# Kernel optimization log

Measured on AMD Instinct MI355X. Metric: run time of the kernel, lower is better.

Reference implementation:

```python
import jax, jax.numpy as jnp
import numpy as np

HEADS = 4
DIM_HEAD = 128


def setup_inputs() -> dict:
    key = jax.random.key(0)
    k1, k2, k3, k4 = jax.random.split(key, 4)
    b, dim, H, W = 4, 256, 128, 128
    hidden = HEADS * DIM_HEAD  # 512
    x = jax.random.normal(k1, (b, dim, H, W), dtype=jnp.float32)
    # 1x1 convs are pointwise matmuls over channels
    w_qkv = jax.random.normal(k2, (hidden * 3, dim), dtype=jnp.float32) * 0.02
    w_out = jax.random.normal(k3, (dim, hidden), dtype=jnp.float32) * 0.02
    b_out = jax.random.normal(k4, (dim,), dtype=jnp.float32) * 0.02
    return {"x": x, "w_qkv": w_qkv, "w_out": w_out, "b_out": b_out}


def reference(x, w_qkv, w_out, b_out):
    b, c, h, w = x.shape
    n = h * w
    # to_qkv: 1x1 conv (no bias) == channel matmul -> [b, 3*heads*dh, h, w]
    qkv = jnp.einsum('bchw,oc->bohw', x, w_qkv)
    # 'b (qkv heads d) h w -> qkv b heads d (h w)'
    qkv = qkv.reshape(b, 3, HEADS, DIM_HEAD, n)
    q, k, v = qkv[:, 0], qkv[:, 1], qkv[:, 2]  # each [b, heads, d, n]
    k = jax.nn.softmax(k, axis=-1)  # softmax over spatial positions
    context = jnp.einsum('bhdn,bhen->bhde', k, v)   # [b, heads, d, d]
    out = jnp.einsum('bhde,bhdn->bhen', context, q)  # [b, heads, d, n]
    out = out.reshape(b, HEADS * DIM_HEAD, h, w)
    # to_out: 1x1 conv with bias
    return jnp.einsum('bchw,oc->bohw', out, w_out) + b_out[None, :, None, None]
```

## Files before the change

### kernel.cpp

```cpp
#include <hip/hip_runtime.h>
#include <hip/hip_bf16.h>

#define HEADS 4
#define DH    128
#define CIN   256
#define NPIX  16384
#define NB    4
#define HID   512

typedef __attribute__((ext_vector_type(8))) short bf16x8;
typedef __attribute__((ext_vector_type(4))) float f32x4;

__device__ __forceinline__ unsigned short f2bfu(float f) {
    union { __hip_bfloat16 h; unsigned short u; } cv;
    cv.h = __float2bfloat16(f);
    return cv.u;
}

typedef const __attribute__((address_space(1))) unsigned char* gas_t;
typedef __attribute__((address_space(3))) unsigned char* las_t;
__device__ __forceinline__ void glds16(const void* g, void* s) {
    __builtin_amdgcn_global_load_lds((gas_t)g, (las_t)s, 16, 0, 0);
}


__global__ __launch_bounds__(256) void xt_convert2(const float* __restrict__ x,
                                                   unsigned short* __restrict__ xt2,
                                                   unsigned short* __restrict__ xbf2)
{
    __shared__ float tile[64][66];
    const int b = blockIdx.z, c0 = blockIdx.y * 64, n0 = blockIdx.x * 64;
    const int t = threadIdx.x, lane = t & 63, wid = t >> 6;
    const float* xb = x + ((size_t)b * CIN + c0) * NPIX + n0;
#pragma unroll
    for (int p = 0; p < 4; ++p) {
        const int c = p * 16 + (t >> 4);
        const int n = (t & 15) * 4;
        float4 v = *reinterpret_cast<const float4*>(xb + (size_t)c * NPIX + n);
        tile[c][n + 0] = v.x; tile[c][n + 1] = v.y;
        tile[c][n + 2] = v.z; tile[c][n + 3] = v.w;
    }
    __syncthreads();
#pragma unroll
    for (int rr = 0; rr < 2; ++rr) {
        const int tid  = wid * 2 + rr;
        const int n16l = tid >> 1, c32l = tid & 1;
        const int nl   = n16l * 16 + (lane & 15);
        const int cb   = c32l * 32 + (lane >> 4) * 8;
        unsigned short u8[8];
#pragma unroll
        for (int j = 0; j < 8; ++j) u8[j] = f2bfu(tile[cb + j][nl]);
        *reinterpret_cast<uint4*>(
            xt2 + (((size_t)b * 1024 + (n0 >> 4) + n16l) * 8 + (c0 >> 5) + c32l) * 512 + lane * 8)
            = *reinterpret_cast<const uint4*>(u8);
    }
#pragma unroll
    for (int rr = 0; rr < 2; ++rr) {
        const int tid  = wid * 2 + rr;
        const int c16l = tid >> 1, n32l = tid & 1;
        const int cr   = c16l * 16 + (lane & 15);
        const int nb   = n32l * 32 + (lane >> 4) * 8;
        unsigned short u8[8];
#pragma unroll
        for (int j = 0; j < 8; ++j) u8[j] = f2bfu(tile[cr][nb + j]);
        *reinterpret_cast<uint4*>(
            xbf2 + (((size_t)b * 16 + (c0 >> 4) + c16l) * 512 + (n0 >> 5) + n32l) * 512 + lane * 8)
            = *reinterpret_cast<const uint4*>(u8);
    }
}

__global__ __launch_bounds__(256) void wconv3(const float* __restrict__ w_qkv,
                                              const float* __restrict__ w_out,
                                              unsigned short* __restrict__ WkF,
                                              unsigned short* __restrict__ WvF,
                                              unsigned short* __restrict__ WqTF,
                                              unsigned short* __restrict__ WoF)
{
    const int t = threadIdx.x, lane = t & 63, wid = t >> 6;
    const int tile = blockIdx.x * 4 + wid;
    unsigned short u8[8];
    unsigned short* dst;
    if (tile < 256) {
        const int h = tile >> 6, d16 = (tile >> 3) & 7, c32 = tile & 7;
        const float* src = w_qkv + (size_t)(512 + h * 128 + d16 * 16 + (lane & 15)) * CIN
                         + c32 * 32 + (lane >> 4) * 8;
#pragma unroll
        for (int j = 0; j < 8; ++j) u8[j] = f2bfu(src[j]);
        dst = WkF + (size_t)tile * 512 + lane * 8;
    } else if (tile < 512) {
        const int t2 = tile - 256;
        const int h = t2 >> 6, e16 = (t2 >> 3) & 7, c32 = t2 & 7;
        const float* src = w_qkv + (size_t)(1024 + h * 128 + e16 * 16 + (lane & 15)) * CIN
                         + c32 * 32 + (lane >> 4) * 8;
#pragma unroll
        for (int j = 0; j < 8; ++j) u8[j] = f2bfu(src[j]);
        dst = WvF + (size_t)t2 * 512 + lane * 8;
    } else if (tile < 768) {
        const int t2 = tile - 512;
        const int h = t2 >> 6, c16 = (t2 >> 2) & 15, d32 = t2 & 3;
#pragma unroll
        for (int j = 0; j < 8; ++j)
            u8[j] = f2bfu(w_qkv[(size_t)(h * 128 + d32 * 32 + (lane >> 4) * 8 + j) * CIN
                                + c16 * 16 + (lane & 15)]);
        dst = WqTF + (size_t)t2 * 512 + lane * 8;
    } else {
        const int t2 = tile - 768;
        const int o16 = t2 >> 4, m32 = t2 & 15;
        const float* src = w_out + (size_t)(o16 * 16 + (lane & 15)) * HID
                         + m32 * 32 + (lane >> 4) * 8;
#pragma unroll
        for (int j = 0; j < 8; ++j) u8[j] = f2bfu(src[j]);
        dst = WoF + (size_t)t2 * 512 + lane * 8;
    }
    *reinterpret_cast<uint4*>(dst) = *reinterpret_cast<const uint4*>(u8);
}

__global__ __launch_bounds__(512, 4) void kg_fused4(const unsigned short* __restrict__ xt2,
                                                    const unsigned short* __restrict__ xbf2,
                                                    const unsigned short* __restrict__ WkF,
                                                    float* __restrict__ G,
                                                    float* __restrict__ S)
{
    __shared__ unsigned short sXT[2][16 * 512];
    __shared__ unsigned short sXB[2][16 * 512];
    __shared__ unsigned short sP[4 * 512];

    const int t = threadIdx.x, lane = t & 63, wid = t >> 6;
    const int ns = blockIdx.x, hd = blockIdx.y, b = blockIdx.z;
    const int h = hd >> 1, dh = hd & 1;
    const int bh = b * 4 + h;
    const int wm = wid >> 1, wn = wid & 1;
    const int wd = wid >> 2, wcq = wid & 3;
    const int cl = lane & 15, r0q = (lane >> 4) * 4;

    bf16x8 aW[8];
#pragma unroll
    for (int ks = 0; ks < 8; ++ks)
        aW[ks] = *reinterpret_cast<const bf16x8*>(
            WkF + ((size_t)((h * 8 + dh * 4 + wm) * 8 + ks)) * 512 + lane * 8);

    f32x4 accG[2][4] = {};
    float Sacc[4] = {};

#define STAGE(nt_, buf_)                                                          \
    {                                                                             \
        _Pragma("unroll")                                                         \
        for (int q = 0; q < 2; ++q) {                                             \
            const int tl = wid * 2 + q;                                           \
            glds16(xt2 + (((size_t)(b * 1024 + ns * 64 + (nt_) * 2 + (tl >> 3))) * 8 \
                          + (tl & 7)) * 512 + lane * 8,                           \
                   sXT[buf_] + (size_t)tl * 512);                                 \
        }                                                                         \
        _Pragma("unroll")                                                         \
        for (int q = 0; q < 2; ++q) {                                             \
            const int tl = wid * 2 + q;                                           \
            glds16(xbf2 + (((size_t)(b * 16 + tl)) * 512 + ns * 32 + (nt_)) * 512 \
                          + lane * 8,                                             \
                   sXB[buf_] + (size_t)tl * 512);                                 \
        }                                                                         \
    }

    STAGE(0, 0);
    __syncthreads();

    int cur = 0;
    for (int nt = 0; nt < 32; ++nt) {
        if (nt < 31) STAGE(nt + 1, cur ^ 1);

        f32x4 acc1 = {};
#pragma unroll
        for (int ks = 0; ks < 8; ++ks) {
            bf16x8 bb = *reinterpret_cast<const bf16x8*>(
                &sXT[cur][(wn * 8 + ks) * 512 + lane * 8]);
            acc1 = __builtin_amdgcn_mfma_f32_16x16x32_bf16(aW[ks], bb, acc1, 0, 0, 0);
        }

#pragma unroll
        for (int r = 0; r < 4; ++r) {
            const float v = __expf(acc1[r]);
            Sacc[r] += v;
            const int us = ((r0q + r) + 16 * (wn * 2 + (cl >> 3))) * 8 + (cl & 7);
            sP[wm * 512 + us] = f2bfu(v);
        }
        __syncthreads();

        {
            const bf16x8 pa0 = *reinterpret_cast<const bf16x8*>(&sP[(wd * 2 + 0) * 512 + lane * 8]);
            const bf16x8 pa1 = *reinterpret_cast<const bf16x8*>(&sP[(wd * 2 + 1) * 512 + lane * 8]);
#pragma unroll
            for (int fj = 0; fj < 4; ++fj) {
                const bf16x8 bb = *reinterpret_cast<const bf16x8*>(
                    &sXB[cur][(wcq * 4 + fj) * 512 + lane * 8]);
                accG[0][fj] = __builtin_amdgcn_mfma_f32_16x16x32_bf16(pa0, bb, accG[0][fj], 0, 0, 0);
                accG[1][fj] = __builtin_amdgcn_mfma_f32_16x16x32_bf16(pa1, bb, accG[1][fj], 0, 0, 0);
            }
        }
        __syncthreads();
        cur ^= 1;
    }
#undef STAGE

#pragma unroll
    for (int r = 0; r < 4; ++r) {
        float v = Sacc[r];
        v += __shfl_xor(v, 1); v += __shfl_xor(v, 2);
        v += __shfl_xor(v, 4); v += __shfl_xor(v, 8);
        if (cl == 0)
            atomicAdd(&S[bh * 128 + dh * 64 + wm * 16 + r0q + r], v);
    }

#pragma unroll
    for (int fi = 0; fi < 2; ++fi)
#pragma unroll
        for (int fj = 0; fj < 4; ++fj)
#pragma unroll
            for (int r = 0; r < 4; ++r) {
                const int d = dh * 64 + wd * 32 + fi * 16 + r0q + r;
                const int c = wcq * 64 + fj * 16 + cl;
                atomicAdd(&G[(size_t)bh * 32768 + d * 256 + c], accG[fi][fj][r]);
            }
}

__global__ __launch_bounds__(256) void c1_kernel(const float* __restrict__ G,
                                                 const float* __restrict__ S,
                                                 const unsigned short* __restrict__ WvF,
                                                 const unsigned short* __restrict__ WqTF,
                                                 unsigned short* __restrict__ AbarF)
{
    __shared__ unsigned short sCtx[32 * 512];
    const int t = threadIdx.x, lane = t & 63, wid = t >> 6;
    const int bh = blockIdx.x, b = bh >> 2, h = bh & 3;
    const int cl = lane & 15, r0q = (lane >> 4) * 4;
    const int wr = wid >> 1, wc = wid & 1;
    const float* Gb = G + (size_t)bh * 32768;

    float invs[4];
#pragma unroll
    for (int fi = 0; fi < 4; ++fi)
        invs[fi] = 1.0f / S[bh * 128 + wr * 64 + fi * 16 + cl];

    f32x4 acc[4][4] = {};
#pragma unroll
    for (int ks = 0; ks < 8; ++ks) {
        bf16x8 a[4], bb[4];
#pragma unroll
        for (int fi = 0; fi < 4; ++fi) {
            const float* gp = Gb + (size_t)(wr * 64 + fi * 16 + cl) * 256
                            + ks * 32 + (lane >> 4) * 8;
            const float4 v0 = *reinterpret_cast<const float4*>(gp);
            const float4 v1 = *reinterpret_cast<const float4*>(gp + 4);
            unsigned short u8[8] = {
                f2bfu(v0.x * invs[fi]), f2bfu(v0.y * invs[fi]),
                f2bfu(v0.z * invs[fi]), f2bfu(v0.w * invs[fi]),
                f2bfu(v1.x * invs[fi]), f2bfu(v1.y * invs[fi]),
                f2bfu(v1.z * invs[fi]), f2bfu(v1.w * invs[fi]) };
            a[fi] = *reinterpret_cast<const bf16x8*>(u8);
        }
#pragma unroll
        for (int fj = 0; fj < 4; ++fj)
            bb[fj] = *reinterpret_cast<const bf16x8*>(
                WvF + ((size_t)(h * 8 + wc * 4 + fj) * 8 + ks) * 512 + lane * 8);
#pragma unroll
        for (int fi = 0; fi < 4; ++fi)
#pragma unroll
            for (int fj = 0; fj < 4; ++fj)
                acc[fi][fj] = __builtin_amdgcn_mfma_f32_16x16x32_bf16(
                    a[fi], bb[fj], acc[fi][fj], 0, 0, 0);
    }

#pragma unroll
    for (int fi = 0; fi < 4; ++fi)
#pragma unroll
        for (int fj = 0; fj < 4; ++fj)
#pragma unroll
            for (int r = 0; r < 4; ++r) {
                const int us = (cl + 16 * ((fi & 1) * 2 + ((r0q + r) >> 3))) * 8 + ((r0q + r) & 7);
                sCtx[((wc * 4 + fj) * 4 + wr * 2 + (fi >> 1)) * 512 + us] = f2bfu(acc[fi][fj][r]);
            }
    __syncthreads();

    const int we = wid >> 1, wcq = wid & 1;
    f32x4 acc2[4][8] = {};
#pragma unroll
    for (int ks = 0; ks < 4; ++ks) {
        bf16x8 a2[4], b2[8];
#pragma unroll
        for (int fi = 0; fi < 4; ++fi)
            a2[fi] = *reinterpret_cast<const bf16x8*>(
                &sCtx[((we * 4 + fi) * 4 + ks) * 512 + lane * 8]);
#pragma unroll
        for (int fj = 0; fj < 8; ++fj)
            b2[fj] = *reinterpret_cast<const bf16x8*>(
                WqTF + ((size_t)(h * 16 + wcq * 8 + fj) * 4 + ks) * 512 + lane * 8);
#pragma unroll
        for (int fi = 0; fi < 4; ++fi)
#pragma unroll
            for (int fj = 0; fj < 8; ++fj)
                acc2[fi][fj] = __builtin_amdgcn_mfma_f32_16x16x32_bf16(
                    a2[fi], b2[fj], acc2[fi][fj], 0, 0, 0);
    }

#pragma unroll
    for (int fi = 0; fi < 4; ++fi)
#pragma unroll
        for (int fj = 0; fj < 8; ++fj)
#pragma unroll
            for (int r = 0; r < 4; ++r) {
                const int c16 = wcq * 8 + fj;
                const int m32 = h * 4 + we * 2 + (fi >> 1);
                const int us  = (cl + 16 * ((fi & 1) * 2 + ((r0q + r) >> 3))) * 8 + ((r0q + r) & 7);
                AbarF[((size_t)(b * 16 + c16) * 16 + m32) * 512 + us] = f2bfu(acc2[fi][fj][r]);
            }
}

__global__ __launch_bounds__(256) void c2_kernel(const unsigned short* __restrict__ WoF,
                                                 const unsigned short* __restrict__ AbarF,
                                                 unsigned short* __restrict__ F2)
{
    const int t = threadIdx.x, lane = t & 63, wid = t >> 6;
    const int csp = blockIdx.x, b = blockIdx.y;
    const int cl = lane & 15, r0q = (lane >> 4) * 4;

    f32x4 acc[4][4] = {};
#pragma unroll
    for (int ks = 0; ks < 16; ++ks) {
        bf16x8 a[4], bb[4];
#pragma unroll
        for (int fi = 0; fi < 4; ++fi)
            a[fi] = *reinterpret_cast<const bf16x8*>(
                WoF + ((size_t)(wid * 4 + fi) * 16 + ks) * 512 + lane * 8);
#pragma unroll
        for (int fj = 0; fj < 4; ++fj)
            bb[fj] = *reinterpret_cast<const bf16x8*>(
                AbarF + ((size_t)(b * 16 + csp * 4 + fj) * 16 + ks) * 512 + lane * 8);
#pragma unroll
        for (int fi = 0; fi < 4; ++fi)
#pragma unroll
            for (int fj = 0; fj < 4; ++fj)
                acc[fi][fj] = __builtin_amdgcn_mfma_f32_16x16x32_bf16(
                    a[fi], bb[fj], acc[fi][fj], 0, 0, 0);
    }

#pragma unroll
    for (int fi = 0; fi < 4; ++fi)
#pragma unroll
        for (int fj = 0; fj < 4; ++fj)
#pragma unroll
            for (int r = 0; r < 4; ++r) {
                const int o16 = wid * 4 + fi;
                const int c32 = csp * 2 + (fj >> 1);
                const int us  = ((r0q + r) + 16 * ((fj & 1) * 2 + (cl >> 3))) * 8 + (cl & 7);
                F2[((size_t)(b * 16 + o16) * 8 + c32) * 512 + us] = f2bfu(acc[fi][fj][r]);
            }
}

__global__ __launch_bounds__(256, 2) void out_gemm3(const unsigned short* __restrict__ xt2,
                                                    const unsigned short* __restrict__ F2,
                                                    const float* __restrict__ b_out,
                                                    float* __restrict__ out)
{
    __shared__ unsigned short sXT[64 * 512];
    const int t = threadIdx.x, lane = t & 63, wid = t >> 6;
    const int n0 = blockIdx.x * 128, m0 = blockIdx.y * 128, b = blockIdx.z;
    const int wr = wid >> 1, wc = wid & 1;

    const unsigned short* src = xt2 + ((size_t)(b * 1024 + (n0 >> 4)) * 8) * 512;
#pragma unroll
    for (int p = 0; p < 16; ++p) {
        const int tl = p * 4 + wid;
        glds16(src + (size_t)tl * 512 + lane * 8, sXT + (size_t)tl * 512);
    }
    __syncthreads();

    f32x4 acc[4][4] = {};
#pragma unroll
    for (int ks = 0; ks < 8; ++ks) {
        bf16x8 a[4], bb[4];
#pragma unroll
        for (int fi = 0; fi < 4; ++fi)
            a[fi] = *reinterpret_cast<const bf16x8*>(
                F2 + (((size_t)b * 16 + (m0 >> 4) + wr * 4 + fi) * 8 + ks) * 512 + lane * 8);
#pragma unroll
        for (int fj = 0; fj < 4; ++fj)
            bb[fj] = *reinterpret_cast<const bf16x8*>(
                &sXT[((wc * 4 + fj) * 8 + ks) * 512 + lane * 8]);
#pragma unroll
        for (int fi = 0; fi < 4; ++fi)
#pragma unroll
            for (int fj = 0; fj < 4; ++fj)
                acc[fi][fj] = __builtin_amdgcn_mfma_f32_16x16x32_bf16(
                    a[fi], bb[fj], acc[fi][fj], 0, 0, 0);
    }

    const int col = lane & 15, r0q = (lane >> 4) * 4;
#pragma unroll
    for (int fi = 0; fi < 4; ++fi)
#pragma unroll
        for (int r = 0; r < 4; ++r) {
            const int o = m0 + wr * 64 + fi * 16 + r0q + r;
            const float bias = b_out[o];
#pragma unroll
            for (int fj = 0; fj < 4; ++fj)
                out[((size_t)b * CIN + o) * NPIX + n0 + wc * 64 + fj * 16 + col] =
                    acc[fi][fj][r] + bias;
        }
}

extern "C" void kernel_launch(void* const* d_in, const int* in_sizes, int n_in,
                              void* d_out, int out_size, void* d_ws, size_t ws_size,
                              hipStream_t stream)
{
    const float* x     = (const float*)d_in[0];
    const float* w_qkv = (const float*)d_in[1];
    const float* w_out = (const float*)d_in[2];
    const float* b_out = (const float*)d_in[3];
    float* out = (float*)d_out;

    char* ws = (char*)d_ws;
    unsigned short* xt2   = (unsigned short*)ws;
    unsigned short* xbf2  = (unsigned short*)(ws + (32ull << 20));
    unsigned short* WkF   = (unsigned short*)(ws + (64ull << 20));
    unsigned short* WvF   = (unsigned short*)(ws + (64ull << 20) + (256u << 10));
    unsigned short* WqTF  = (unsigned short*)(ws + (64ull << 20) + (512u << 10));
    unsigned short* WoF   = (unsigned short*)(ws + (64ull << 20) + (768u << 10));
    float*          S     = (float*)(ws + (65ull << 20));
    float*          G     = (float*)(ws + (66ull << 20));
    unsigned short* AbarF = (unsigned short*)(ws + (68ull << 20));
    unsigned short* F2    = (unsigned short*)(ws + (69ull << 20));

    hipMemsetAsync(S, 0, 2048 * sizeof(float), stream);
    hipMemsetAsync(G, 0, (size_t)16 * 32768 * sizeof(float), stream);
    xt_convert2<<<dim3(NPIX / 64, CIN / 64, NB), 256, 0, stream>>>(x, xt2, xbf2);
    wconv3<<<256, 256, 0, stream>>>(w_qkv, w_out, WkF, WvF, WqTF, WoF);
    kg_fused4<<<dim3(16, 8, NB), 512, 0, stream>>>(xt2, xbf2, WkF, G, S);
    c1_kernel<<<16, 256, 0, stream>>>(G, S, WvF, WqTF, AbarF);
    c2_kernel<<<dim3(4, NB), 256, 0, stream>>>(WoF, AbarF, F2);
    out_gemm3<<<dim3(NPIX / 128, CIN / 128, NB), 256, 0, stream>>>(xt2, F2, b_out, out);
}
```

Before: 150.2 us.

## Give each wave a full 16-row k-slice so exp tile stays wave-private

```diff
diff --git a/kernel.cpp b/kernel.cpp
--- a/kernel.cpp
+++ b/kernel.cpp
@@ -115,7 +115,7 @@
     *reinterpret_cast<uint4*>(dst) = *reinterpret_cast<const uint4*>(u8);
 }
 
-__global__ __launch_bounds__(512, 4) void kg_fused4(const unsigned short* __restrict__ xt2,
+__global__ __launch_bounds__(512, 4) void kg_fused5(const unsigned short* __restrict__ xt2,
                                                     const unsigned short* __restrict__ xbf2,
                                                     const unsigned short* __restrict__ WkF,
                                                     float* __restrict__ G,
@@ -123,38 +123,35 @@
 {
     __shared__ unsigned short sXT[2][16 * 512];
     __shared__ unsigned short sXB[2][16 * 512];
-    __shared__ unsigned short sP[4 * 512];
-
-    const int t = threadIdx.x, lane = t & 63, wid = t >> 6;
-    const int ns = blockIdx.x, hd = blockIdx.y, b = blockIdx.z;
-    const int h = hd >> 1, dh = hd & 1;
+    __shared__ unsigned short sP[8 * 512];
+
+    const int t = threadIdx.x, lane = t & 63, wid = t >> 6;
+    const int ns = blockIdx.x, h = blockIdx.y, b = blockIdx.z;
     const int bh = b * 4 + h;
-    const int wm = wid >> 1, wn = wid & 1;
-    const int wd = wid >> 2, wcq = wid & 3;
-    const int cl = lane & 15, r0q = (lane >> 4) * 4;
+    const int q = lane >> 4, cl = lane & 15;
 
     bf16x8 aW[8];
 #pragma unroll
     for (int ks = 0; ks < 8; ++ks)
         aW[ks] = *reinterpret_cast<const bf16x8*>(
-            WkF + ((size_t)((h * 8 + dh * 4 + wm) * 8 + ks)) * 512 + lane * 8);
-
-    f32x4 accG[2][4] = {};
-    float Sacc[4] = {};
+            WkF + ((size_t)((h * 8 + wid) * 8 + ks)) * 512 + lane * 8);
+
+    f32x4 accG[16] = {};
+    float Sacc = 0.f;
 
 #define STAGE(nt_, buf_)                                                          \
     {                                                                             \
         _Pragma("unroll")                                                         \
-        for (int q = 0; q < 2; ++q) {                                             \
-            const int tl = wid * 2 + q;                                           \
-            glds16(xt2 + (((size_t)(b * 1024 + ns * 64 + (nt_) * 2 + (tl >> 3))) * 8 \
+        for (int q2 = 0; q2 < 2; ++q2) {                                          \
+            const int tl = wid * 2 + q2;             \
+            glds16(xt2 + (((size_t)(b * 1024 + ns * 32 + (nt_) * 2 + (tl >> 3))) * 8 \
                           + (tl & 7)) * 512 + lane * 8,                           \
                    sXT[buf_] + (size_t)tl * 512);                                 \
         }                                                                         \
         _Pragma("unroll")                                                         \
-        for (int q = 0; q < 2; ++q) {                                             \
-            const int tl = wid * 2 + q;                                           \
-            glds16(xbf2 + (((size_t)(b * 16 + tl)) * 512 + ns * 32 + (nt_)) * 512 \
+        for (int q2 = 0; q2 < 2; ++q2) {                                          \
+            const int tl = wid * 2 + q2;                            \
+            glds16(xbf2 + (((size_t)(b * 16 + tl)) * 512 + ns * 16 + (nt_)) * 512 \
                           + lane * 8,                                             \
                    sXB[buf_] + (size_t)tl * 512);                                 \
         }                                                                         \
@@ -164,61 +161,62 @@
     __syncthreads();
 
     int cur = 0;
-    for (int nt = 0; nt < 32; ++nt) {
-        if (nt < 31) STAGE(nt + 1, cur ^ 1);
-
-        f32x4 acc1 = {};
+    for (int nt = 0; nt < 16; ++nt) {
+        if (nt < 15) STAGE(nt + 1, cur ^ 1);
+
+        f32x4 acc1[2] = {};
 #pragma unroll
         for (int ks = 0; ks < 8; ++ks) {
-            bf16x8 bb = *reinterpret_cast<const bf16x8*>(
-                &sXT[cur][(wn * 8 + ks) * 512 + lane * 8]);
-            acc1 = __builtin_amdgcn_mfma_f32_16x16x32_bf16(aW[ks], bb, acc1, 0, 0, 0);
+            const bf16x8 a0 = *reinterpret_cast<const bf16x8*>(
+                &sXT[cur][(0 * 8 + ks) * 512 + lane * 8]);
+            const bf16x8 a1 = *reinterpret_cast<const bf16x8*>(
+                &sXT[cur][(1 * 8 + ks) * 512 + lane * 8]);
+            acc1[0] = __builtin_amdgcn_mfma_f32_16x16x32_bf16(a0, aW[ks], acc1[0], 0, 0, 0);
+            acc1[1] = __builtin_amdgcn_mfma_f32_16x16x32_bf16(a1, aW[ks], acc1[1], 0, 0, 0);
         }
 
-#pragma unroll
-        for (int r = 0; r < 4; ++r) {
-            const float v = __expf(acc1[r]);
-            Sacc[r] += v;
-            const int us = ((r0q + r) + 16 * (wn * 2 + (cl >> 3))) * 8 + (cl & 7);
-            sP[wm * 512 + us] = f2bfu(v);
+        unsigned* sPw = reinterpret_cast<unsigned*>(&sP[wid * 512]);
+#pragma unroll
+        for (int s = 0; s < 2; ++s)
+#pragma unroll
+            for (int p = 0; p < 2; ++p) {
+                const float e0 = __expf(acc1[s][2 * p]);
+                const float e1 = __expf(acc1[s][2 * p + 1]);
+                Sacc += e0 + e1;
+                const unsigned pk = (unsigned)f2bfu(e0) | ((unsigned)f2bfu(e1) << 16);
+                const int us = (cl + 16 * (2 * s + (q >> 1))) * 8 + (q & 1) * 4 + 2 * p;
+                sPw[us >> 1] = pk;
+            }
+        const bf16x8 pa = *reinterpret_cast<const bf16x8*>(&sP[wid * 512 + lane * 8]);
+
+#pragma unroll
+        for (int fj = 0; fj < 16; ++fj) {
+            const bf16x8 bb = *reinterpret_cast<const bf16x8*>(
+                &sXB[cur][fj * 512 + lane * 8]);
+            accG[fj] = __builtin_amdgcn_mfma_f32_16x16x32_bf16(pa, bb, accG[fj], 0, 0, 0);
         }
-        __syncthreads();
-
-        {
-            const bf16x8 pa0 = *reinterpret_cast<const bf16x8*>(&sP[(wd * 2 + 0) * 512 + lane * 8]);
-            const bf16x8 pa1 = *reinterpret_cast<const bf16x8*>(&sP[(wd * 2 + 1) * 512 + lane * 8]);
-#pragma unroll
-            for (int fj = 0; fj < 4; ++fj) {
-                const bf16x8 bb = *reinterpret_cast<const bf16x8*>(
-                    &sXB[cur][(wcq * 4 + fj) * 512 + lane * 8]);
-                accG[0][fj] = __builtin_amdgcn_mfma_f32_16x16x32_bf16(pa0, bb, accG[0][fj], 0, 0, 0);
-                accG[1][fj] = __builtin_amdgcn_mfma_f32_16x16x32_bf16(pa1, bb, accG[1][fj], 0, 0, 0);
-            }
-        }
+
         __syncthreads();
         cur ^= 1;
     }
 #undef STAGE
 
-#pragma unroll
-    for (int r = 0; r < 4; ++r) {
-        float v = Sacc[r];
-        v += __shfl_xor(v, 1); v += __shfl_xor(v, 2);
-        v += __shfl_xor(v, 4); v += __shfl_xor(v, 8);
-        if (cl == 0)
-            atomicAdd(&S[bh * 128 + dh * 64 + wm * 16 + r0q + r], v);
-    }
-
-#pragma unroll
-    for (int fi = 0; fi < 2; ++fi)
-#pragma unroll
-        for (int fj = 0; fj < 4; ++fj)
-#pragma unroll
-            for (int r = 0; r < 4; ++r) {
-                const int d = dh * 64 + wd * 32 + fi * 16 + r0q + r;
-                const int c = wcq * 64 + fj * 16 + cl;
-                atomicAdd(&G[(size_t)bh * 32768 + d * 256 + c], accG[fi][fj][r]);
-            }
+    {
+        float v = Sacc;
+        v += __shfl_xor(v, 16);
+        v += __shfl_xor(v, 32);
+        if (lane < 16)
+            atomicAdd(&S[bh * 128 + wid * 16 + lane], v);
+    }
+
+#pragma unroll
+    for (int fj = 0; fj < 16; ++fj)
+#pragma unroll
+        for (int r = 0; r < 4; ++r) {
+            const int d = wid * 16 + q * 4 + r;
+            const int c = fj * 16 + cl;
+            atomicAdd(&G[(size_t)bh * 32768 + d * 256 + c], accG[fj][r]);
+        }
 }
 
 __global__ __launch_bounds__(256) void c1_kernel(const float* __restrict__ G,
@@ -432,7 +430,7 @@
     hipMemsetAsync(G, 0, (size_t)16 * 32768 * sizeof(float), stream);
     xt_convert2<<<dim3(NPIX / 64, CIN / 64, NB), 256, 0, stream>>>(x, xt2, xbf2);
     wconv3<<<256, 256, 0, stream>>>(w_qkv, w_out, WkF, WvF, WqTF, WoF);
-    kg_fused4<<<dim3(16, 8, NB), 512, 0, stream>>>(xt2, xbf2, WkF, G, S);
+    kg_fused5<<<dim3(32, HEADS, NB), 512, 0, stream>>>(xt2, xbf2, WkF, G, S);
     c1_kernel<<<16, 256, 0, stream>>>(G, S, WvF, WqTF, AbarF);
     c2_kernel<<<dim3(4, NB), 256, 0, stream>>>(WoF, AbarF, F2);
     out_gemm3<<<dim3(NPIX / 128, CIN / 128, NB), 256, 0, stream>>>(xt2, F2, b_out, out);
```

New measurement: 171.9 us. 1.14x slower.

## Merge head-dim halves into one block with larger tiles and XCD-aware grid mapping

Applied to the files above, without the earlier changes.

```diff
diff --git a/kernel.cpp b/kernel.cpp
--- a/kernel.cpp
+++ b/kernel.cpp
@@ -115,107 +115,149 @@
     *reinterpret_cast<uint4*>(dst) = *reinterpret_cast<const uint4*>(u8);
 }
 
-__global__ __launch_bounds__(512, 4) void kg_fused4(const unsigned short* __restrict__ xt2,
+__global__ __launch_bounds__(512, 2) void kg_fused6(const unsigned short* __restrict__ xt2,
                                                     const unsigned short* __restrict__ xbf2,
                                                     const unsigned short* __restrict__ WkF,
                                                     float* __restrict__ G,
                                                     float* __restrict__ S)
 {
-    __shared__ unsigned short sXT[2][16 * 512];
-    __shared__ unsigned short sXB[2][16 * 512];
-    __shared__ unsigned short sP[4 * 512];
-
-    const int t = threadIdx.x, lane = t & 63, wid = t >> 6;
-    const int ns = blockIdx.x, hd = blockIdx.y, b = blockIdx.z;
-    const int h = hd >> 1, dh = hd & 1;
-    const int bh = b * 4 + h;
+    __shared__ unsigned short sXT[2][32 * 512];
+    __shared__ unsigned short sXB[2][32 * 512];
+    __shared__ unsigned short sP[16 * 512];
+
+    const int wgid = blockIdx.x;
+    const int xcd  = wgid & 7;
+    const int k_   = wgid >> 3;
+    const int h    = k_ & 3;
+    const int g_   = xcd + 8 * (k_ >> 2);
+    const int ns   = g_ & 15;
+    const int b    = g_ >> 4;
+    const int bh   = b * 4 + h;
+
+    const int t = threadIdx.x, lane = t & 63, wid = t >> 6;
     const int wm = wid >> 1, wn = wid & 1;
     const int wd = wid >> 2, wcq = wid & 3;
     const int cl = lane & 15, r0q = (lane >> 4) * 4;
 
-    bf16x8 aW[8];
-#pragma unroll
-    for (int ks = 0; ks < 8; ++ks)
-        aW[ks] = *reinterpret_cast<const bf16x8*>(
-            WkF + ((size_t)((h * 8 + dh * 4 + wm) * 8 + ks)) * 512 + lane * 8);
-
-    f32x4 accG[2][4] = {};
-    float Sacc[4] = {};
-
-#define STAGE(nt_, buf_)                                                          \
-    {                                                                             \
-        _Pragma("unroll")                                                         \
-        for (int q = 0; q < 2; ++q) {                                             \
-            const int tl = wid * 2 + q;                                           \
-            glds16(xt2 + (((size_t)(b * 1024 + ns * 64 + (nt_) * 2 + (tl >> 3))) * 8 \
-                          + (tl & 7)) * 512 + lane * 8,                           \
-                   sXT[buf_] + (size_t)tl * 512);                                 \
-        }                                                                         \
-        _Pragma("unroll")                                                         \
-        for (int q = 0; q < 2; ++q) {                                             \
-            const int tl = wid * 2 + q;                                           \
-            glds16(xbf2 + (((size_t)(b * 16 + tl)) * 512 + ns * 32 + (nt_)) * 512 \
-                          + lane * 8,                                             \
-                   sXB[buf_] + (size_t)tl * 512);                                 \
-        }                                                                         \
-    }
-
-    STAGE(0, 0);
+    bf16x8 aW[2][8];
+#pragma unroll
+    for (int fi = 0; fi < 2; ++fi)
+#pragma unroll
+        for (int ks = 0; ks < 8; ++ks)
+            aW[fi][ks] = *reinterpret_cast<const bf16x8*>(
+                WkF + ((size_t)(h * 64 + (wm * 2 + fi) * 8 + ks)) * 512 + lane * 8);
+
+    f32x4 accG[4][4] = {};
+    float Sacc[8] = {};
+
+    const unsigned short* xtb = xt2 + ((size_t)(b * 1024 + ns * 64) * 8) * 512;
+
+#define STAGE_XT(nt_, buf_)                                                     \
+    {                                                                           \
+        const unsigned short* src_ = xtb + (size_t)(nt_) * 4 * 8 * 512;         \
+        _Pragma("unroll")                                                       \
+        for (int p = 0; p < 4; ++p) {                                           \
+            const int tl = p * 8 + wid;                                         \
+            glds16(src_ + (size_t)tl * 512 + lane * 8, sXT[buf_] + (size_t)tl * 512); \
+        }                                                                       \
+    }
+#define STAGE_XB(nt_, buf_)                                                     \
+    {                                                                           \
+        const size_t nb32_ = (size_t)ns * 32 + (nt_) * 2;                       \
+        _Pragma("unroll")                                                       \
+        for (int p = 0; p < 4; ++p) {                                           \
+            const int tl = p * 8 + wid;                                         \
+            const int c16_ = tl >> 1, n32l_ = tl & 1;                           \
+            glds16(xbf2 + (((size_t)(b * 16 + c16_)) * 512 + nb32_ + n32l_) * 512 + lane * 8, \
+                   sXB[buf_] + (size_t)tl * 512);                               \
+        }                                                                       \
+    }
+
+    STAGE_XT(0, 0);
+    STAGE_XB(0, 0);
     __syncthreads();
 
     int cur = 0;
-    for (int nt = 0; nt < 32; ++nt) {
-        if (nt < 31) STAGE(nt + 1, cur ^ 1);
-
-        f32x4 acc1 = {};
+    for (int nt = 0; nt < 16; ++nt) {
+        if (nt < 15) {
+            STAGE_XT(nt + 1, cur ^ 1);
+            STAGE_XB(nt + 1, cur ^ 1);
+        }
+
+        f32x4 acc1[2][2] = {};
 #pragma unroll
         for (int ks = 0; ks < 8; ++ks) {
-            bf16x8 bb = *reinterpret_cast<const bf16x8*>(
-                &sXT[cur][(wn * 8 + ks) * 512 + lane * 8]);
-            acc1 = __builtin_amdgcn_mfma_f32_16x16x32_bf16(aW[ks], bb, acc1, 0, 0, 0);
-        }
-
-#pragma unroll
-        for (int r = 0; r < 4; ++r) {
-            const float v = __expf(acc1[r]);
-            Sacc[r] += v;
-            const int us = ((r0q + r) + 16 * (wn * 2 + (cl >> 3))) * 8 + (cl & 7);
-            sP[wm * 512 + us] = f2bfu(v);
-        }
+            bf16x8 bb[2];
+#pragma unroll
+            for (int fj = 0; fj < 2; ++fj)
+                bb[fj] = *reinterpret_cast<const bf16x8*>(
+                    &sXT[cur][((wn * 2 + fj) * 8 + ks) * 512 + lane * 8]);
+#pragma unroll
+            for (int fi = 0; fi < 2; ++fi)
+#pragma unroll
+                for (int fj = 0; fj < 2; ++fj)
+                    acc1[fi][fj] = __builtin_amdgcn_mfma_f32_16x16x32_bf16(
+                        aW[fi][ks], bb[fj], acc1[fi][fj], 0, 0, 0);
+        }
+
+#pragma unroll
+        for (int fi = 0; fi < 2; ++fi)
+#pragma unroll
+            for (int r = 0; r < 4; ++r) {
+                float rs = 0.f;
+#pragma unroll
+                for (int fj = 0; fj < 2; ++fj) {
+                    const float v = __expf(acc1[fi][fj][r]);
+                    rs += v;
+                    const int us = ((r0q + r) + 16 * (fj * 2 + (cl >> 3))) * 8 + (cl & 7);
+                    sP[((wm * 2 + fi) * 2 + wn) * 512 + us] = f2bfu(v);
+                }
+                Sacc[fi * 4 + r] += rs;
+            }
         __syncthreads();
 
-        {
-            const bf16x8 pa0 = *reinterpret_cast<const bf16x8*>(&sP[(wd * 2 + 0) * 512 + lane * 8]);
-            const bf16x8 pa1 = *reinterpret_cast<const bf16x8*>(&sP[(wd * 2 + 1) * 512 + lane * 8]);
-#pragma unroll
-            for (int fj = 0; fj < 4; ++fj) {
-                const bf16x8 bb = *reinterpret_cast<const bf16x8*>(
-                    &sXB[cur][(wcq * 4 + fj) * 512 + lane * 8]);
-                accG[0][fj] = __builtin_amdgcn_mfma_f32_16x16x32_bf16(pa0, bb, accG[0][fj], 0, 0, 0);
-                accG[1][fj] = __builtin_amdgcn_mfma_f32_16x16x32_bf16(pa1, bb, accG[1][fj], 0, 0, 0);
-            }
+#pragma unroll
+        for (int kn = 0; kn < 2; ++kn) {
+            bf16x8 pa[4], bb[4];
+#pragma unroll
+            for (int fi = 0; fi < 4; ++fi)
+                pa[fi] = *reinterpret_cast<const bf16x8*>(
+                    &sP[((wd * 4 + fi) * 2 + kn) * 512 + lane * 8]);
+#pragma unroll
+            for (int fj = 0; fj < 4; ++fj)
+                bb[fj] = *reinterpret_cast<const bf16x8*>(
+                    &sXB[cur][((wcq * 4 + fj) * 2 + kn) * 512 + lane * 8]);
+#pragma unroll
+            for (int fi = 0; fi < 4; ++fi)
+#pragma unroll
+                for (int fj = 0; fj < 4; ++fj)
+                    accG[fi][fj] = __builtin_amdgcn_mfma_f32_16x16x32_bf16(
+                        pa[fi], bb[fj], accG[fi][fj], 0, 0, 0);
         }
         __syncthreads();
         cur ^= 1;
     }
-#undef STAGE
-
-#pragma unroll
-    for (int r = 0; r < 4; ++r) {
-        float v = Sacc[r];
+#undef STAGE_XT
+#undef STAGE_XB
+
+#pragma unroll
+    for (int i = 0; i < 8; ++i) {
+        float v = Sacc[i];
         v += __shfl_xor(v, 1); v += __shfl_xor(v, 2);
         v += __shfl_xor(v, 4); v += __shfl_xor(v, 8);
-        if (cl == 0)
-            atomicAdd(&S[bh * 128 + dh * 64 + wm * 16 + r0q + r], v);
-    }
-
-#pragma unroll
-    for (int fi = 0; fi < 2; ++fi)
+        if (cl == 0) {
+            const int d = wm * 32 + (i >> 2) * 16 + r0q + (i & 3);
+            atomicAdd(&S[bh * 128 + d], v);
+        }
+    }
+
+#pragma unroll
+    for (int fi = 0; fi < 4; ++fi)
 #pragma unroll
         for (int fj = 0; fj < 4; ++fj)
 #pragma unroll
             for (int r = 0; r < 4; ++r) {
-                const int d = dh * 64 + wd * 32 + fi * 16 + r0q + r;
+                const int d = wd * 64 + fi * 16 + r0q + r;
                 const int c = wcq * 64 + fj * 16 + cl;
                 atomicAdd(&G[(size_t)bh * 32768 + d * 256 + c], accG[fi][fj][r]);
             }
@@ -432,7 +474,7 @@
     hipMemsetAsync(G, 0, (size_t)16 * 32768 * sizeof(float), stream);
     xt_convert2<<<dim3(NPIX / 64, CIN / 64, NB), 256, 0, stream>>>(x, xt2, xbf2);
     wconv3<<<256, 256, 0, stream>>>(w_qkv, w_out, WkF, WvF, WqTF, WoF);
-    kg_fused4<<<dim3(16, 8, NB), 512, 0, stream>>>(xt2, xbf2, WkF, G, S);
+    kg_fused6<<<256, 512, 0, stream>>>(xt2, xbf2, WkF, G, S);
     c1_kernel<<<16, 256, 0, stream>>>(G, S, WvF, WqTF, AbarF);
     c2_kernel<<<dim3(4, NB), 256, 0, stream>>>(WoF, AbarF, F2);
     out_gemm3<<<dim3(NPIX / 128, CIN / 128, NB), 256, 0, stream>>>(xt2, F2, b_out, out);
```

Measured after the change: 149.7 us. About the same (-0.3%).
